# Optimization experiments

Hardware: AMD Instinct MI355X
Metric: run time of the kernel (lower is better)

## Reference

```python
import jax, jax.numpy as jnp
import numpy as np

SIGMA = 8.0
C_SIZE = 512
STRIDE = 8
BG_RATIO = 0.15
EPS = 1e-5


def setup_inputs() -> dict:
    key = jax.random.key(0)
    k1, k2 = jax.random.split(key)
    B, N = 16, 512
    # head-point coordinates uniformly in the crop [0, C_SIZE)
    points = jax.random.uniform(k1, (B, N, 2), dtype=jnp.float32) * C_SIZE
    # per-image shortest side sizes, realistic crop scales
    st_sizes = jax.random.uniform(k2, (B,), dtype=jnp.float32) * 256.0 + 256.0
    return {"points": points, "st_sizes": st_sizes}


def reference(points, st_sizes):
    # pixel-center coordinates of the downsampled density grid, [C]
    cood = jnp.arange(0, C_SIZE, STRIDE, dtype=jnp.float32) + STRIDE / 2.0
    B, N, _ = points.shape
    C = cood.shape[0]
    x = points[..., 0]  # [B, N]
    y = points[..., 1]  # [B, N]
    # (x - c)^2 == -2*x*c + x^2 + c^2 (the matmul trick in the original)
    x_dis = (x[..., None] - cood) ** 2  # [B, N, C]
    y_dis = (y[..., None] - cood) ** 2  # [B, N, C]
    # dis[b, p, i, j] = (y_p - cood_i)^2 + (x_p - cood_j)^2
    dis = y_dis[:, :, :, None] + x_dis[:, :, None, :]  # [B, N, C, C]
    dis = dis.reshape(B, N, C * C)  # [B, N, M]
    # background distance: per-pixel min over points, clamped at 0
    min_dis = jnp.clip(jnp.min(dis, axis=1, keepdims=True), 0.0)  # [B, 1, M]
    bg_dis = (st_sizes[:, None, None] * BG_RATIO) ** 2 / (min_dis + EPS)
    dis = jnp.concatenate([dis, bg_dis], axis=1)  # [B, N+1, M]
    logits = -dis / (2.0 * SIGMA ** 2)
    # softmax over the point (+background) axis, per pixel
    return jax.nn.softmax(logits, axis=1)
```

## Files before the change

kernel.cpp:

```cpp
#include <hip/hip_runtime.h>
#include <hip/hip_bf16.h>
#include <cstddef>

constexpr int NPT = 512;
constexpr int C   = 64;
constexpr int M   = C * C;
constexpr int NP1 = NPT + 1;
constexpr float K = 1.0f / 128.0f;
constexpr float BG_RATIO = 0.15f;
constexpr float EPS = 1e-5f;

__global__ __launch_bounds__(256) void pp_kernel(
    const float* __restrict__ points,
    const float* __restrict__ st,
    float* __restrict__ out)
{
    const int b    = blockIdx.x >> 6;
    const int i    = blockIdx.x & 63;
    const int t    = threadIdx.x;
    const int lane = t & 63;
    const int w    = t >> 6;
    const int jg   = t & 15;
    const int pc   = t >> 4;

    const float cy  = (float)(i * 8 + 4);
    const float cx0 = (float)(jg * 32 + 4);
    const float cx1 = cx0 + 8.0f;
    const float cx2 = cx0 + 16.0f;
    const float cx3 = cx0 + 24.0f;

    __shared__ float2 pts[NPT];
    __shared__ float4 redmin[4][16];
    __shared__ float4 redsum[4][16];
    __shared__ float  rs[C];
    __shared__ float  bgs[C];

    const float2* pb = (const float2*)(points + (size_t)b * NPT * 2);
    for (int p = t; p < NPT; p += 256) pts[p] = pb[p];
    __syncthreads();

    const int p0 = pc * 32;

    float4 mn = make_float4(3.4e38f, 3.4e38f, 3.4e38f, 3.4e38f);
    float4 sm = make_float4(0.f, 0.f, 0.f, 0.f);
    #pragma unroll 4
    for (int k = 0; k < 32; ++k) {
        float2 xy = pts[p0 + k];
        float dy  = xy.y - cy;
        float dy2 = dy * dy;
        float dx0 = xy.x - cx0, dx1 = xy.x - cx1, dx2 = xy.x - cx2, dx3 = xy.x - cx3;
        float d0 = fmaf(dx0, dx0, dy2);
        float d1 = fmaf(dx1, dx1, dy2);
        float d2 = fmaf(dx2, dx2, dy2);
        float d3 = fmaf(dx3, dx3, dy2);
        mn.x = fminf(mn.x, d0); mn.y = fminf(mn.y, d1);
        mn.z = fminf(mn.z, d2); mn.w = fminf(mn.w, d3);
        sm.x += __expf(-d0 * K); sm.y += __expf(-d1 * K);
        sm.z += __expf(-d2 * K); sm.w += __expf(-d3 * K);
    }

    #pragma unroll
    for (int off = 16; off <= 32; off <<= 1) {
        mn.x = fminf(mn.x, __shfl_xor(mn.x, off));
        mn.y = fminf(mn.y, __shfl_xor(mn.y, off));
        mn.z = fminf(mn.z, __shfl_xor(mn.z, off));
        mn.w = fminf(mn.w, __shfl_xor(mn.w, off));
        sm.x += __shfl_xor(sm.x, off);
        sm.y += __shfl_xor(sm.y, off);
        sm.z += __shfl_xor(sm.z, off);
        sm.w += __shfl_xor(sm.w, off);
    }
    if (lane < 16) { redmin[w][lane] = mn; redsum[w][lane] = sm; }
    __syncthreads();

    if (t < C) {
        const float* rm = (const float*)redmin;
        const float* rq = (const float*)redsum;
        float m0 = fminf(fminf(rm[t], rm[64 + t]), fminf(rm[128 + t], rm[192 + t]));
        float s0 = (rq[t] + rq[64 + t]) + (rq[128 + t] + rq[192 + t]);
        float ss = st[b] * BG_RATIO;
        float bg = (ss * ss) / (m0 + EPS);
        float tot = s0 + __expf(-bg * K);
        bgs[t] = bg;
        rs[t]  = 1.0f / tot;
    }
    __syncthreads();

    const float4 r4 = *(const float4*)&rs[jg * 4];

    float* ob = out + (size_t)b * NP1 * M + (size_t)p0 * M + i * C + jg * 4;
    #pragma unroll 4
    for (int k = 0; k < 32; ++k) {
        float2 xy = pts[p0 + k];
        float dy  = xy.y - cy;
        float dy2 = dy * dy;
        float dx0 = xy.x - cx0, dx1 = xy.x - cx1, dx2 = xy.x - cx2, dx3 = xy.x - cx3;
        float4 v;
        v.x = __expf(-fmaf(dx0, dx0, dy2) * K) * r4.x;
        v.y = __expf(-fmaf(dx1, dx1, dy2) * K) * r4.y;
        v.z = __expf(-fmaf(dx2, dx2, dy2) * K) * r4.z;
        v.w = __expf(-fmaf(dx3, dx3, dy2) * K) * r4.w;
        *(float4*)(ob + (size_t)k * M) = v;
    }

    if (t < C) {
        out[(size_t)b * NP1 * M + (size_t)NPT * M + i * C + t] =
            __expf(-bgs[t] * K) * rs[t];
    }
}

extern "C" void kernel_launch(void* const* d_in, const int* in_sizes, int n_in,
                              void* d_out, int out_size, void* d_ws, size_t ws_size,
                              hipStream_t stream) {
    const float* points = (const float*)d_in[0];
    const float* st     = (const float*)d_in[1];
    float* out          = (float*)d_out;

    const int B = in_sizes[1];
    dim3 grid(B * C);
    dim3 block(256);
    pp_kernel<<<grid, block, 0, stream>>>(points, st, out);
}
```

Measured before the change: 140.3 us.

## Split into denominator and write kernels with contiguous nontemporal output stores

```diff
diff --git a/kernel.cpp b/kernel.cpp
--- a/kernel.cpp
+++ b/kernel.cpp
@@ -1,19 +1,21 @@
 #include <hip/hip_runtime.h>
-#include <hip/hip_bf16.h>
 #include <cstddef>
 
 constexpr int NPT = 512;
 constexpr int C   = 64;
 constexpr int M   = C * C;
 constexpr int NP1 = NPT + 1;
-constexpr float K = 1.0f / 128.0f;
 constexpr float BG_RATIO = 0.15f;
 constexpr float EPS = 1e-5f;
+constexpr float NEGK2 = -0.0112710550069450f;
 
-__global__ __launch_bounds__(256) void pp_kernel(
+typedef float f4 __attribute__((ext_vector_type(4)));
+
+__global__ __launch_bounds__(256) void denom_kernel(
     const float* __restrict__ points,
     const float* __restrict__ st,
-    float* __restrict__ out)
+    float* __restrict__ out,
+    float* __restrict__ rsw)
 {
     const int b    = blockIdx.x >> 6;
     const int i    = blockIdx.x & 63;
@@ -32,8 +34,6 @@
     __shared__ float2 pts[NPT];
     __shared__ float4 redmin[4][16];
     __shared__ float4 redsum[4][16];
-    __shared__ float  rs[C];
-    __shared__ float  bgs[C];
 
     const float2* pb = (const float2*)(points + (size_t)b * NPT * 2);
     for (int p = t; p < NPT; p += 256) pts[p] = pb[p];
@@ -55,8 +55,8 @@
         float d3 = fmaf(dx3, dx3, dy2);
         mn.x = fminf(mn.x, d0); mn.y = fminf(mn.y, d1);
         mn.z = fminf(mn.z, d2); mn.w = fminf(mn.w, d3);
-        sm.x += __expf(-d0 * K); sm.y += __expf(-d1 * K);
-        sm.z += __expf(-d2 * K); sm.w += __expf(-d3 * K);
+        sm.x += exp2f(d0 * NEGK2); sm.y += exp2f(d1 * NEGK2);
+        sm.z += exp2f(d2 * NEGK2); sm.w += exp2f(d3 * NEGK2);
     }
 
     #pragma unroll
@@ -80,32 +80,53 @@
         float s0 = (rq[t] + rq[64 + t]) + (rq[128 + t] + rq[192 + t]);
         float ss = st[b] * BG_RATIO;
         float bg = (ss * ss) / (m0 + EPS);
-        float tot = s0 + __expf(-bg * K);
-        bgs[t] = bg;
-        rs[t]  = 1.0f / tot;
+        float eb = exp2f(bg * NEGK2);
+        float r  = 1.0f / (s0 + eb);
+        rsw[(size_t)b * M + i * C + t] = r;
+        out[(size_t)b * NP1 * M + (size_t)NPT * M + i * C + t] = eb * r;
     }
-    __syncthreads();
+}
 
-    const float4 r4 = *(const float4*)&rs[jg * 4];
+__global__ __launch_bounds__(256) void write_kernel(
+    const float* __restrict__ points,
+    const float* __restrict__ rsw,
+    float* __restrict__ out)
+{
+    const int b   = blockIdx.x >> 6;
+    const int pch = blockIdx.x & 63;
+    const int t   = threadIdx.x;
 
-    float* ob = out + (size_t)b * NP1 * M + (size_t)p0 * M + i * C + jg * 4;
-    #pragma unroll 4
-    for (int k = 0; k < 32; ++k) {
-        float2 xy = pts[p0 + k];
-        float dy  = xy.y - cy;
-        float dy2 = dy * dy;
-        float dx0 = xy.x - cx0, dx1 = xy.x - cx1, dx2 = xy.x - cx2, dx3 = xy.x - cx3;
-        float4 v;
-        v.x = __expf(-fmaf(dx0, dx0, dy2) * K) * r4.x;
-        v.y = __expf(-fmaf(dx1, dx1, dy2) * K) * r4.y;
-        v.z = __expf(-fmaf(dx2, dx2, dy2) * K) * r4.z;
-        v.w = __expf(-fmaf(dx3, dx3, dy2) * K) * r4.w;
-        *(float4*)(ob + (size_t)k * M) = v;
+    float cyv[4], cxv[4];
+    f4 r4[4];
+    #pragma unroll
+    for (int q = 0; q < 4; ++q) {
+        int m4 = (q * 256 + t) * 4;
+        cyv[q] = (float)((m4 >> 6) * 8 + 4);
+        cxv[q] = (float)((m4 & 63) * 8 + 4);
+        r4[q]  = *(const f4*)(rsw + (size_t)b * M + m4);
     }
 
-    if (t < C) {
-        out[(size_t)b * NP1 * M + (size_t)NPT * M + i * C + t] =
-            __expf(-bgs[t] * K) * rs[t];
+    const float2* pb = (const float2*)(points + (size_t)b * NPT * 2) + pch * 8;
+    float* ob = out + (size_t)b * NP1 * M + (size_t)(pch * 8) * M + t * 4;
+
+    #pragma unroll 2
+    for (int p = 0; p < 8; ++p) {
+        const float x = pb[p].x;
+        const float y = pb[p].y;
+        float* op = ob + (size_t)p * M;
+        #pragma unroll
+        for (int q = 0; q < 4; ++q) {
+            float dy  = y - cyv[q];
+            float dy2 = dy * dy;
+            float dx0 = x - cxv[q];
+            float dx1 = dx0 - 8.0f, dx2 = dx0 - 16.0f, dx3 = dx0 - 24.0f;
+            f4 v;
+            v.x = exp2f(fmaf(dx0, dx0, dy2) * NEGK2) * r4[q].x;
+            v.y = exp2f(fmaf(dx1, dx1, dy2) * NEGK2) * r4[q].y;
+            v.z = exp2f(fmaf(dx2, dx2, dy2) * NEGK2) * r4[q].z;
+            v.w = exp2f(fmaf(dx3, dx3, dy2) * NEGK2) * r4[q].w;
+            __builtin_nontemporal_store(v, (f4*)(op + q * 1024));
+        }
     }
 }
 
@@ -115,9 +136,9 @@
     const float* points = (const float*)d_in[0];
     const float* st     = (const float*)d_in[1];
     float* out          = (float*)d_out;
+    float* rsw          = (float*)d_ws;
 
     const int B = in_sizes[1];
-    dim3 grid(B * C);
-    dim3 block(256);
-    pp_kernel<<<grid, block, 0, stream>>>(points, st, out);
+    denom_kernel<<<dim3(B * C), dim3(256), 0, stream>>>(points, st, out, rsw);
+    write_kernel<<<dim3(B * C), dim3(256), 0, stream>>>(points, rsw, out);
 }
```

Result: slower. 155.3 us (+10.7%).
